# Kernel tuning notes

Measured on AMD Instinct MI355X. Metric: run time of the kernel, lower is better.

Reference implementation:

```python
import jax, jax.numpy as jnp
from jax import lax
import numpy as np

B, CIN, COUT, H, W = 4, 64, 64, 128, 128
K = 3      # kernel size
G = 1      # groups (== offset groups)
PAD = 1
STRIDE = 1


def setup_inputs() -> dict:
    key = jax.random.key(0)
    k1, k2, k3 = jax.random.split(key, 3)
    x = jax.random.normal(k1, (B, CIN, H, W), jnp.float32)
    # offset-predicting conv weight: (2*G*K*K, CIN, K, K); small init like real nets
    w_offset = jax.random.normal(k2, (2 * G * K * K, CIN, K, K), jnp.float32) * 0.01
    # deformable conv weight: (COUT, CIN//G, K, K)
    w_deform = jax.random.normal(k3, (COUT, CIN // G, K, K), jnp.float32) * (1.0 / np.sqrt(CIN * K * K))
    return {"x": x, "w_offset": w_offset, "w_deform": w_deform}


def _deform_conv2d(x, w_offset, w_deform):
    Bn, C, Hi, Wi = x.shape
    K2 = K * K
    Cg = C // G
    # 1) predict offsets with a plain conv
    offset = lax.conv_general_dilated(
        x, w_offset, (STRIDE, STRIDE), [(PAD, PAD), (PAD, PAD)],
        dimension_numbers=("NCHW", "OIHW", "NCHW"))
    Ho, Wo = offset.shape[2], offset.shape[3]
    # torchvision layout: channel 2*(g*K2 + i*K + j) = dy, +1 = dx
    off = offset.reshape(Bn, G, K2, 2, Ho, Wo)
    dy = off[:, :, :, 0]  # (B,G,K2,Ho,Wo)
    dx = off[:, :, :, 1]
    # base sampling grid
    ky = jnp.repeat(jnp.arange(K), K).astype(x.dtype)  # (K2,) kernel row offsets
    kx = jnp.tile(jnp.arange(K), K).astype(x.dtype)    # (K2,) kernel col offsets
    base_y = (jnp.arange(Ho) * STRIDE - PAD).astype(x.dtype)[:, None]   # (Ho,1)
    base_x = (jnp.arange(Wo) * STRIDE - PAD).astype(x.dtype)[None, :]   # (1,Wo)
    py = base_y[None, None, None] + ky[None, None, :, None, None] + dy  # (B,G,K2,Ho,Wo)
    px = base_x[None, None, None] + kx[None, None, :, None, None] + dx
    # 2) bilinear sampling with zero padding outside the image
    y0 = jnp.floor(py)
    x0 = jnp.floor(px)
    ly = py - y0
    lx = px - x0
    y0i = y0.astype(jnp.int32)
    x0i = x0.astype(jnp.int32)
    xr = x.reshape(Bn, G, Cg, Hi, Wi)

    def corner(yi, xi, wgt):
        valid = ((yi >= 0) & (yi < Hi) & (xi >= 0) & (xi < Wi)).astype(x.dtype)
        yc = jnp.clip(yi, 0, Hi - 1)
        xc = jnp.clip(xi, 0, Wi - 1)
        # gather per (batch, group): xg[:, yy, xx] -> (Cg, K2, Ho, Wo)
        g = jax.vmap(jax.vmap(lambda xg, yy, xx: xg[:, yy, xx]))(xr, yc, xc)
        return g * (wgt * valid)[:, :, None]  # broadcast over Cg

    v = (corner(y0i,     x0i,     (1 - ly) * (1 - lx))
         + corner(y0i,     x0i + 1, (1 - ly) * lx)
         + corner(y0i + 1, x0i,     ly * (1 - lx))
         + corner(y0i + 1, x0i + 1, ly * lx))  # (B,G,Cg,K2,Ho,Wo)
    # 3) grouped contraction with the deformable conv weight
    wr = w_deform.reshape(G, COUT // G, Cg, K2)
    out = jnp.einsum('bgckhw,gock->bgohw', v, wr)
    return out.reshape(Bn, COUT, Ho, Wo)


def reference(x, w_offset, w_deform):
    return _deform_conv2d(x, w_offset, w_deform)
```

## Files before the change

kernel.cpp:

```cpp
#include <hip/hip_runtime.h>

#define B_    4
#define CIN_  64
#define COUT_ 64
#define H_    128
#define W_    128
#define HW_   (H_*W_)
#define K2_   9
#define NOFF_ 18

#define PR_   132
#define PC_   136
#define TROWS 5
#define TCOLS 70
#define NSEG  (TROWS * 8 * TCOLS)
#define NSEGP 2816

typedef _Float16 f16x8 __attribute__((ext_vector_type(8)));
typedef float    f32x4 __attribute__((ext_vector_type(4)));

__device__ __forceinline__ f16x8 splat8(float f) {
    _Float16 h = (_Float16)f;
    return (f16x8){h, h, h, h, h, h, h, h};
}
__device__ __forceinline__ f16x8 splat8h(_Float16 h) {
    return (f16x8){h, h, h, h, h, h, h, h};
}
__device__ __forceinline__ _Float16 lo16(unsigned u) {
    return __builtin_bit_cast(_Float16, (unsigned short)(u & 0xffffu));
}
__device__ __forceinline__ _Float16 hi16(unsigned u) {
    return __builtin_bit_cast(_Float16, (unsigned short)(u >> 16));
}

#define NW_B   (COUT_ * 576)
#define NW_OB  (32 * 576)
#define NBORD  (4 * 12544)
__global__ __launch_bounds__(256) void x2h_prep(const float* __restrict__ x,
                                                const float* __restrict__ wd,
                                                const float* __restrict__ wo,
                                                _Float16* __restrict__ hx,
                                                _Float16* __restrict__ wt_b,
                                                _Float16* __restrict__ wt_ob) {
    const int blk = blockIdx.x;
    const int b = blk >> 7, y = blk & 127;
    const int xp = threadIdx.x & 127;
    const int ch = threadIdx.x >> 7;
    const float* xs = x + ((b * CIN_ + ch * 32) * H_ + y) * W_ + xp;
    _Float16* hd = hx + (((size_t)b * PR_ + y + 2) * PC_ + xp + 3) * 64 + ch * 32;

    f16x8 h[4];
    #pragma unroll
    for (int j = 0; j < 4; ++j)
        #pragma unroll
        for (int t = 0; t < 8; ++t)
            h[j][t] = (_Float16)xs[(j * 8 + t) * HW_];
    #pragma unroll
    for (int j = 0; j < 4; ++j)
        *(f16x8*)(hd + j * 8) = h[j];

    const int gid = blk * 256 + threadIdx.x;
    if (gid < NW_B) {
        int blk512 = gid >> 9, w = gid & 511;
        int nl = w >> 5, cc = w & 31;
        int kb = blk512 & 1, t = blk512 >> 1;
        int mb = t / 9, k2 = t - 9 * mb;
        int o = mb * 16 + nl, c = kb * 32 + cc;
        wt_b[gid] = (_Float16)wd[(o * CIN_ + c) * K2_ + k2];
    } else if (gid < NW_B + NW_OB) {
        int u = gid - NW_B;
        int blk512 = u >> 9, w = u & 511;
        int nl = w >> 5, cc = w & 31;
        int kb = blk512 & 1, t = blk512 >> 1;
        int mt = t / 9, k2 = t - 9 * mt;
        int oc = mt * 16 + nl, c = kb * 32 + cc;
        wt_ob[u] = (_Float16)((oc < NOFF_) ? wo[(oc * CIN_ + c) * K2_ + k2] : 0.f);
    } else if (gid < NW_B + NW_OB + NBORD) {
        int s = gid - (NW_B + NW_OB);
        int b2 = s / 12544, u = s % 12544;
        int cs = u & 7, cell = u >> 3;
        int r, c;
        if (cell < 544) {
            int r4 = cell / 136; c = cell % 136;
            r = (r4 < 2) ? r4 : r4 + 128;
        } else {
            int c2 = cell - 544;
            r = 2 + (c2 >> 3);
            int c8 = c2 & 7;
            c = (c8 < 3) ? c8 : c8 + 128;
        }
        *(f16x8*)(hx + (((size_t)b2 * PR_ + r) * PC_ + c) * 64 + cs * 8) = splat8(0.f);
    }
}

__global__ __launch_bounds__(256, 3) void deform_all(const _Float16* __restrict__ hx,
                                                     const _Float16* __restrict__ wt_b,
                                                     const _Float16* __restrict__ wt_ob,
                                                     float* __restrict__ out) {
    __shared__ __align__(16) _Float16 xt[NSEGP * 8];

    const int tid = threadIdx.x;
    int blk = blockIdx.x;
    blk = (blk & 7) * 128 + (blk >> 3);
    const int b   = blk >> 8;
    const int r2  = blk & 255;
    const int oh  = r2 >> 1;
    const int ow0 = (r2 & 1) << 6;

    const _Float16* hrow = hx + (((size_t)b * PR_ + oh) * PC_ + ow0) * 64;
    #pragma unroll
    for (int t = 0; t < NSEGP / 256; ++t) {
        int d  = t * 256 + tid;
        int dc = min(d, NSEG - 1);
        int col = dc % TCOLS;
        int rc  = dc / TCOLS;
        int cs  = rc & 7;
        int r   = rc >> 3;
        const _Float16* src = hrow + ((size_t)r * PC_ + col) * 64 + cs * 8;
        __builtin_amdgcn_global_load_lds(
            (const __attribute__((address_space(1))) void*)src,
            (__attribute__((address_space(3))) void*)(xt + (size_t)d * 8),
            16, 0, 0);
    }

    const int lane = tid & 63;
    const int cq   = tid >> 6;
    const int quad = lane >> 4;
    const int nl   = lane & 15;
    const int pix  = cq * 16 + nl;
    const int ow   = ow0 + pix;

    const _Float16* wob_l = wt_ob + nl * 32 + quad * 8;
    const _Float16* wtb_l = wt_b  + nl * 32 + quad * 8;
    const _Float16* hb    = hx + (size_t)b * (PR_ * PC_ * 64);

    f32x4 oacc[2];
    oacc[0] = (f32x4){0.f, 0.f, 0.f, 0.f};
    oacc[1] = (f32x4){0.f, 0.f, 0.f, 0.f};
    #pragma unroll
    for (int t9 = 0; t9 < 9; ++t9) {
        int ky = t9 / 3, kx = t9 - 3 * (t9 / 3);
        #pragma unroll
        for (int kb = 0; kb < 2; ++kb) {
            f16x8 bfr = *(const f16x8*)(hb + (((oh + ky + 1) * PC_) + (ow + kx + 2)) * 64
                                           + kb * 32 + quad * 8);
            #pragma unroll
            for (int mt = 0; mt < 2; ++mt) {
                f16x8 afr = *(const f16x8*)(wob_l + (((mt * 9 + t9) * 2 + kb) << 9));
                oacc[mt] = __builtin_amdgcn_mfma_f32_16x16x32_f16(afr, bfr, oacc[mt], 0, 0, 0);
            }
        }
    }

    float dyv[9], dxv[9];
    #pragma unroll
    for (int k2 = 0; k2 < 9; ++k2) {
        const int oc0 = 2 * k2;
        const int mt  = oc0 >> 4;
        const int sq  = (oc0 & 15) >> 2;
        const int r0  = oc0 & 3;
        dyv[k2] = __shfl(oacc[mt][r0],     sq * 16 + nl, 64);
        dxv[k2] = __shfl(oacc[mt][r0 + 1], sq * 16 + nl, 64);
    }

    int      A00[9];
    unsigned Wp[9][2];
    int      P0[9];
    unsigned okm = 0, dxm = 0, dym = 0;
    #pragma unroll
    for (int k2 = 0; k2 < 9; ++k2) {
        const int ky = k2 / 3, kx = k2 - 3 * (k2 / 3);
        float py = (float)(oh - 1 + ky) + dyv[k2];
        float px = (float)(ow - 1 + kx) + dxv[k2];
        float y0f = floorf(py), x0f = floorf(px);
        float ly = py - y0f,    lx = px - x0f;
        int   y0 = (int)y0f,    x0 = (int)x0f;
        int   y1 = y0 + 1,      x1 = x0 + 1;

        float wy0 = 1.f - ly, wx0 = 1.f - lx;
        float w00 = wy0 * wx0, w01 = wy0 * lx, w10 = ly * wx0, w11 = ly * lx;

        bool vy0 = (unsigned)y0 < (unsigned)H_;
        bool vy1 = (unsigned)y1 < (unsigned)H_;
        bool vx0 = (unsigned)x0 < (unsigned)W_;
        bool vx1 = (unsigned)x1 < (unsigned)W_;
        if (!(vy0 & vx0)) w00 = 0.f;
        if (!(vy0 & vx1)) w01 = 0.f;
        if (!(vy1 & vx0)) w10 = 0.f;
        if (!(vy1 & vx1)) w11 = 0.f;
        unsigned h00 = (unsigned)__builtin_bit_cast(unsigned short, (_Float16)w00);
        unsigned h01 = (unsigned)__builtin_bit_cast(unsigned short, (_Float16)w01);
        unsigned h10 = (unsigned)__builtin_bit_cast(unsigned short, (_Float16)w10);
        unsigned h11 = (unsigned)__builtin_bit_cast(unsigned short, (_Float16)w11);
        Wp[k2][0] = h00 | (h01 << 16);
        Wp[k2][1] = h10 | (h11 << 16);
        P0[k2] = (y0 & 0xffff) | (x0 << 16);

        int ty0 = y0 - (oh - 2), ty1 = ty0 + 1;
        int tx0 = x0 - (ow0 - 3), tx1 = tx0 + 1;
        bool i00 = (unsigned)ty0 < TROWS && (unsigned)tx0 < TCOLS;
        bool i01 = (unsigned)ty0 < TROWS && (unsigned)tx1 < TCOLS;
        bool i10 = (unsigned)ty1 < TROWS && (unsigned)tx0 < TCOLS;
        bool i11 = (unsigned)ty1 < TROWS && (unsigned)tx1 < TCOLS;
        bool ok = (w00 == 0.f || i00) && (w01 == 0.f || i01) &&
                  (w10 == 0.f || i10) && (w11 == 0.f || i11);
        if (ok) okm |= 1u << k2;

        int tyc0 = min(max(ty0, 0), TROWS - 1), tyc1 = min(max(ty1, 0), TROWS - 1);
        int txc0 = min(max(tx0, 0), TCOLS - 1), txc1 = min(max(tx1, 0), TCOLS - 1);
        if (txc1 != txc0) dxm |= 1u << k2;
        if (tyc1 != tyc0) dym |= 1u << k2;
        A00[k2] = ((tyc0 * 8 + quad) * TCOLS + txc0) * 8;
    }

    __syncthreads();

    f32x4 acc[4];
    #pragma unroll
    for (int mb = 0; mb < 4; ++mb) acc[mb] = (f32x4){0.f, 0.f, 0.f, 0.f};

    const int KB1 = 4 * TCOLS * 8;

    #pragma unroll
    for (int k2 = 0; k2 < 9; ++k2) {
        f16x8 af0[4], af1[4];
        #pragma unroll
        for (int mb = 0; mb < 4; ++mb) {
            af0[mb] = *(const f16x8*)(wtb_l + (((mb * 9 + k2) * 2 + 0) << 9));
            af1[mb] = *(const f16x8*)(wtb_l + (((mb * 9 + k2) * 2 + 1) << 9));
        }

        const int a00 = A00[k2];
        const int a01 = a00 + (int)((dxm >> k2) & 1u) * 8;
        const int a10 = a00 + (int)((dym >> k2) & 1u) * (8 * TCOLS * 8);
        const int a11 = a10 + (a01 - a00);
        f16x8 c00a = *(const f16x8*)&xt[a00], c00b = *(const f16x8*)&xt[a00 + KB1];
        f16x8 c01a = *(const f16x8*)&xt[a01], c01b = *(const f16x8*)&xt[a01 + KB1];
        f16x8 c10a = *(const f16x8*)&xt[a10], c10b = *(const f16x8*)&xt[a10 + KB1];
        f16x8 c11a = *(const f16x8*)&xt[a11], c11b = *(const f16x8*)&xt[a11 + KB1];

        f16x8 W00 = splat8h(lo16(Wp[k2][0])), W01 = splat8h(hi16(Wp[k2][0]));
        f16x8 W10 = splat8h(lo16(Wp[k2][1])), W11 = splat8h(hi16(Wp[k2][1]));

        f16x8 v0 = c00a * W00 + c01a * W01 + c10a * W10 + c11a * W11;
        f16x8 v1 = c00b * W00 + c01b * W01 + c10b * W10 + c11b * W11;

        if (!((okm >> k2) & 1u)) {
            int pk = P0[k2];
            int y0 = (pk << 16) >> 16;
            int x0 = pk >> 16;
            int y0c = min(max(y0, 0), H_ - 1), y1c = min(max(y0 + 1, 0), H_ - 1);
            int x0c = min(max(x0, 0), W_ - 1), x1c = min(max(x0 + 1, 0), W_ - 1);
            const _Float16* hg = hb + quad * 8;
            const _Float16* g00 = hg + (((y0c + 2) * PC_) + x0c + 3) * 64;
            const _Float16* g01 = hg + (((y0c + 2) * PC_) + x1c + 3) * 64;
            const _Float16* g10 = hg + (((y1c + 2) * PC_) + x0c + 3) * 64;
            const _Float16* g11 = hg + (((y1c + 2) * PC_) + x1c + 3) * 64;
            v0 = (*(const f16x8*)g00) * W00 + (*(const f16x8*)g01) * W01 +
                 (*(const f16x8*)g10) * W10 + (*(const f16x8*)g11) * W11;
            v1 = (*(const f16x8*)(g00 + 32)) * W00 + (*(const f16x8*)(g01 + 32)) * W01 +
                 (*(const f16x8*)(g10 + 32)) * W10 + (*(const f16x8*)(g11 + 32)) * W11;
        }

        __builtin_amdgcn_s_setprio(1);
        #pragma unroll
        for (int mb = 0; mb < 4; ++mb) {
            acc[mb] = __builtin_amdgcn_mfma_f32_16x16x32_f16(af0[mb], v0, acc[mb], 0, 0, 0);
            acc[mb] = __builtin_amdgcn_mfma_f32_16x16x32_f16(af1[mb], v1, acc[mb], 0, 0, 0);
        }
        __builtin_amdgcn_s_setprio(0);
    }

    #pragma unroll
    for (int mb = 0; mb < 4; ++mb)
        #pragma unroll
        for (int r = 0; r < 4; ++r) {
            int o = mb * 16 + quad * 4 + r;
            out[(b * COUT_ + o) * HW_ + oh * W_ + ow0 + pix] = acc[mb][r];
        }
}

extern "C" void kernel_launch(void* const* d_in, const int* in_sizes, int n_in,
                              void* d_out, int out_size, void* d_ws, size_t ws_size,
                              hipStream_t stream) {
    const float* x        = (const float*)d_in[0];
    const float* w_offset = (const float*)d_in[1];
    const float* w_deform = (const float*)d_in[2];
    float* out = (float*)d_out;

    _Float16* hx    = (_Float16*)d_ws;
    _Float16* wt_b  = hx + (size_t)B_ * PR_ * PC_ * 64;
    _Float16* wt_ob = wt_b + (size_t)NW_B;

    x2h_prep<<<B_ * H_, 256, 0, stream>>>(x, w_deform, w_offset, hx, wt_b, wt_ob);
    deform_all<<<B_ * H_ * (W_ / 64), 256, 0, stream>>>(hx, wt_b, wt_ob, out);
}
```

Baseline: 116.6 us.

## Halve block size, give each wave two pixel groups, read offset-conv input from LDS

Blocks drop from 256 to 128 threads, so each wave now handles 32 pixels as two 16-pixel groups. The A-fragment weight loads for both the offset conv and the deform contraction are shared across the two groups. The offset conv now reads its B operands from the LDS tile instead of global memory, which requires a barrier right after the async tile load. In exchange it uses more registers per thread and loses the overlap that previously hid the tile load behind the offset conv and coordinate math, and occupancy bounds change.

```diff
diff --git a/kernel.cpp b/kernel.cpp
--- a/kernel.cpp
+++ b/kernel.cpp
@@ -93,7 +93,7 @@
     }
 }
 
-__global__ __launch_bounds__(256, 3) void deform_all(const _Float16* __restrict__ hx,
+__global__ __launch_bounds__(128, 2) void deform_all(const _Float16* __restrict__ hx,
                                                      const _Float16* __restrict__ wt_b,
                                                      const _Float16* __restrict__ wt_ob,
                                                      float* __restrict__ out) {
@@ -109,8 +109,8 @@
 
     const _Float16* hrow = hx + (((size_t)b * PR_ + oh) * PC_ + ow0) * 64;
     #pragma unroll
-    for (int t = 0; t < NSEGP / 256; ++t) {
-        int d  = t * 256 + tid;
+    for (int t = 0; t < NSEGP / 128; ++t) {
+        int d  = t * 128 + tid;
         int dc = min(d, NSEG - 1);
         int col = dc % TCOLS;
         int rc  = dc / TCOLS;
@@ -122,102 +122,109 @@
             (__attribute__((address_space(3))) void*)(xt + (size_t)d * 8),
             16, 0, 0);
     }
+    __syncthreads();
 
     const int lane = tid & 63;
     const int cq   = tid >> 6;
     const int quad = lane >> 4;
     const int nl   = lane & 15;
-    const int pix  = cq * 16 + nl;
-    const int ow   = ow0 + pix;
 
     const _Float16* wob_l = wt_ob + nl * 32 + quad * 8;
     const _Float16* wtb_l = wt_b  + nl * 32 + quad * 8;
     const _Float16* hb    = hx + (size_t)b * (PR_ * PC_ * 64);
 
-    f32x4 oacc[2];
-    oacc[0] = (f32x4){0.f, 0.f, 0.f, 0.f};
-    oacc[1] = (f32x4){0.f, 0.f, 0.f, 0.f};
+    f32x4 oacc[2][2];
+    #pragma unroll
+    for (int mt = 0; mt < 2; ++mt)
+        #pragma unroll
+        for (int pg = 0; pg < 2; ++pg)
+            oacc[mt][pg] = (f32x4){0.f, 0.f, 0.f, 0.f};
     #pragma unroll
     for (int t9 = 0; t9 < 9; ++t9) {
         int ky = t9 / 3, kx = t9 - 3 * (t9 / 3);
         #pragma unroll
         for (int kb = 0; kb < 2; ++kb) {
-            f16x8 bfr = *(const f16x8*)(hb + (((oh + ky + 1) * PC_) + (ow + kx + 2)) * 64
-                                           + kb * 32 + quad * 8);
+            f16x8 afr[2];
             #pragma unroll
-            for (int mt = 0; mt < 2; ++mt) {
-                f16x8 afr = *(const f16x8*)(wob_l + (((mt * 9 + t9) * 2 + kb) << 9));
-                oacc[mt] = __builtin_amdgcn_mfma_f32_16x16x32_f16(afr, bfr, oacc[mt], 0, 0, 0);
+            for (int mt = 0; mt < 2; ++mt)
+                afr[mt] = *(const f16x8*)(wob_l + (((mt * 9 + t9) * 2 + kb) << 9));
+            #pragma unroll
+            for (int pg = 0; pg < 2; ++pg) {
+                const int pix = cq * 32 + pg * 16 + nl;
+                f16x8 bfr = *(const f16x8*)&xt[((((ky + 1) * 8) + kb * 4 + quad) * TCOLS + pix + kx + 2) * 8];
+                #pragma unroll
+                for (int mt = 0; mt < 2; ++mt)
+                    oacc[mt][pg] = __builtin_amdgcn_mfma_f32_16x16x32_f16(afr[mt], bfr, oacc[mt][pg], 0, 0, 0);
             }
         }
     }
 
-    float dyv[9], dxv[9];
-    #pragma unroll
-    for (int k2 = 0; k2 < 9; ++k2) {
-        const int oc0 = 2 * k2;
-        const int mt  = oc0 >> 4;
-        const int sq  = (oc0 & 15) >> 2;
-        const int r0  = oc0 & 3;
-        dyv[k2] = __shfl(oacc[mt][r0],     sq * 16 + nl, 64);
-        dxv[k2] = __shfl(oacc[mt][r0 + 1], sq * 16 + nl, 64);
-    }
-
-    int      A00[9];
-    unsigned Wp[9][2];
-    int      P0[9];
-    unsigned okm = 0, dxm = 0, dym = 0;
-    #pragma unroll
-    for (int k2 = 0; k2 < 9; ++k2) {
-        const int ky = k2 / 3, kx = k2 - 3 * (k2 / 3);
-        float py = (float)(oh - 1 + ky) + dyv[k2];
-        float px = (float)(ow - 1 + kx) + dxv[k2];
-        float y0f = floorf(py), x0f = floorf(px);
-        float ly = py - y0f,    lx = px - x0f;
-        int   y0 = (int)y0f,    x0 = (int)x0f;
-        int   y1 = y0 + 1,      x1 = x0 + 1;
-
-        float wy0 = 1.f - ly, wx0 = 1.f - lx;
-        float w00 = wy0 * wx0, w01 = wy0 * lx, w10 = ly * wx0, w11 = ly * lx;
-
-        bool vy0 = (unsigned)y0 < (unsigned)H_;
-        bool vy1 = (unsigned)y1 < (unsigned)H_;
-        bool vx0 = (unsigned)x0 < (unsigned)W_;
-        bool vx1 = (unsigned)x1 < (unsigned)W_;
-        if (!(vy0 & vx0)) w00 = 0.f;
-        if (!(vy0 & vx1)) w01 = 0.f;
-        if (!(vy1 & vx0)) w10 = 0.f;
-        if (!(vy1 & vx1)) w11 = 0.f;
-        unsigned h00 = (unsigned)__builtin_bit_cast(unsigned short, (_Float16)w00);
-        unsigned h01 = (unsigned)__builtin_bit_cast(unsigned short, (_Float16)w01);
-        unsigned h10 = (unsigned)__builtin_bit_cast(unsigned short, (_Float16)w10);
-        unsigned h11 = (unsigned)__builtin_bit_cast(unsigned short, (_Float16)w11);
-        Wp[k2][0] = h00 | (h01 << 16);
-        Wp[k2][1] = h10 | (h11 << 16);
-        P0[k2] = (y0 & 0xffff) | (x0 << 16);
-
-        int ty0 = y0 - (oh - 2), ty1 = ty0 + 1;
-        int tx0 = x0 - (ow0 - 3), tx1 = tx0 + 1;
-        bool i00 = (unsigned)ty0 < TROWS && (unsigned)tx0 < TCOLS;
-        bool i01 = (unsigned)ty0 < TROWS && (unsigned)tx1 < TCOLS;
-        bool i10 = (unsigned)ty1 < TROWS && (unsigned)tx0 < TCOLS;
-        bool i11 = (unsigned)ty1 < TROWS && (unsigned)tx1 < TCOLS;
-        bool ok = (w00 == 0.f || i00) && (w01 == 0.f || i01) &&
-                  (w10 == 0.f || i10) && (w11 == 0.f || i11);
-        if (ok) okm |= 1u << k2;
-
-        int tyc0 = min(max(ty0, 0), TROWS - 1), tyc1 = min(max(ty1, 0), TROWS - 1);
-        int txc0 = min(max(tx0, 0), TCOLS - 1), txc1 = min(max(tx1, 0), TCOLS - 1);
-        if (txc1 != txc0) dxm |= 1u << k2;
-        if (tyc1 != tyc0) dym |= 1u << k2;
-        A00[k2] = ((tyc0 * 8 + quad) * TCOLS + txc0) * 8;
-    }
-
-    __syncthreads();
-
-    f32x4 acc[4];
-    #pragma unroll
-    for (int mb = 0; mb < 4; ++mb) acc[mb] = (f32x4){0.f, 0.f, 0.f, 0.f};
+    int      A00[2][9];
+    unsigned Wp[2][9][2];
+    int      P0[2][9];
+    unsigned okm[2] = {0, 0}, dxm[2] = {0, 0}, dym[2] = {0, 0};
+    #pragma unroll
+    for (int pg = 0; pg < 2; ++pg) {
+        const int ow = ow0 + cq * 32 + pg * 16 + nl;
+        #pragma unroll
+        for (int k2 = 0; k2 < 9; ++k2) {
+            const int oc0 = 2 * k2;
+            const int mt  = oc0 >> 4;
+            const int sq  = (oc0 & 15) >> 2;
+            const int r0  = oc0 & 3;
+            float dy = __shfl(oacc[mt][pg][r0],     sq * 16 + nl, 64);
+            float dx = __shfl(oacc[mt][pg][r0 + 1], sq * 16 + nl, 64);
+
+            const int ky = k2 / 3, kx = k2 - 3 * (k2 / 3);
+            float py = (float)(oh - 1 + ky) + dy;
+            float px = (float)(ow - 1 + kx) + dx;
+            float y0f = floorf(py), x0f = floorf(px);
+            float ly = py - y0f,    lx = px - x0f;
+            int   y0 = (int)y0f,    x0 = (int)x0f;
+            int   y1 = y0 + 1,      x1 = x0 + 1;
+
+            float wy0 = 1.f - ly, wx0 = 1.f - lx;
+            float w00 = wy0 * wx0, w01 = wy0 * lx, w10 = ly * wx0, w11 = ly * lx;
+
+            bool vy0 = (unsigned)y0 < (unsigned)H_;
+            bool vy1 = (unsigned)y1 < (unsigned)H_;
+            bool vx0 = (unsigned)x0 < (unsigned)W_;
+            bool vx1 = (unsigned)x1 < (unsigned)W_;
+            if (!(vy0 & vx0)) w00 = 0.f;
+            if (!(vy0 & vx1)) w01 = 0.f;
+            if (!(vy1 & vx0)) w10 = 0.f;
+            if (!(vy1 & vx1)) w11 = 0.f;
+            unsigned h00 = (unsigned)__builtin_bit_cast(unsigned short, (_Float16)w00);
+            unsigned h01 = (unsigned)__builtin_bit_cast(unsigned short, (_Float16)w01);
+            unsigned h10 = (unsigned)__builtin_bit_cast(unsigned short, (_Float16)w10);
+            unsigned h11 = (unsigned)__builtin_bit_cast(unsigned short, (_Float16)w11);
+            Wp[pg][k2][0] = h00 | (h01 << 16);
+            Wp[pg][k2][1] = h10 | (h11 << 16);
+            P0[pg][k2] = (y0 & 0xffff) | (x0 << 16);
+
+            int ty0 = y0 - (oh - 2), ty1 = ty0 + 1;
+            int tx0 = x0 - (ow0 - 3), tx1 = tx0 + 1;
+            bool i00 = (unsigned)ty0 < TROWS && (unsigned)tx0 < TCOLS;
+            bool i01 = (unsigned)ty0 < TROWS && (unsigned)tx1 < TCOLS;
+            bool i10 = (unsigned)ty1 < TROWS && (unsigned)tx0 < TCOLS;
+            bool i11 = (unsigned)ty1 < TROWS && (unsigned)tx1 < TCOLS;
+            bool ok = (w00 == 0.f || i00) && (w01 == 0.f || i01) &&
+                      (w10 == 0.f || i10) && (w11 == 0.f || i11);
+            if (ok) okm[pg] |= 1u << k2;
+
+            int tyc0 = min(max(ty0, 0), TROWS - 1), tyc1 = min(max(ty1, 0), TROWS - 1);
+            int txc0 = min(max(tx0, 0), TCOLS - 1), txc1 = min(max(tx1, 0), TCOLS - 1);
+            if (txc1 != txc0) dxm[pg] |= 1u << k2;
+            if (tyc1 != tyc0) dym[pg] |= 1u << k2;
+            A00[pg][k2] = ((tyc0 * 8 + quad) * TCOLS + txc0) * 8;
+        }
+    }
+
+    f32x4 acc[2][4];
+    #pragma unroll
+    for (int pg = 0; pg < 2; ++pg)
+        #pragma unroll
+        for (int mb = 0; mb < 4; ++mb) acc[pg][mb] = (f32x4){0.f, 0.f, 0.f, 0.f};
 
     const int KB1 = 4 * TCOLS * 8;
 
@@ -230,54 +237,59 @@
             af1[mb] = *(const f16x8*)(wtb_l + (((mb * 9 + k2) * 2 + 1) << 9));
         }
 
-        const int a00 = A00[k2];
-        const int a01 = a00 + (int)((dxm >> k2) & 1u) * 8;
-        const int a10 = a00 + (int)((dym >> k2) & 1u) * (8 * TCOLS * 8);
-        const int a11 = a10 + (a01 - a00);
-        f16x8 c00a = *(const f16x8*)&xt[a00], c00b = *(const f16x8*)&xt[a00 + KB1];
-        f16x8 c01a = *(const f16x8*)&xt[a01], c01b = *(const f16x8*)&xt[a01 + KB1];
-        f16x8 c10a = *(const f16x8*)&xt[a10], c10b = *(const f16x8*)&xt[a10 + KB1];
-        f16x8 c11a = *(const f16x8*)&xt[a11], c11b = *(const f16x8*)&xt[a11 + KB1];
-
-        f16x8 W00 = splat8h(lo16(Wp[k2][0])), W01 = splat8h(hi16(Wp[k2][0]));
-        f16x8 W10 = splat8h(lo16(Wp[k2][1])), W11 = splat8h(hi16(Wp[k2][1]));
-
-        f16x8 v0 = c00a * W00 + c01a * W01 + c10a * W10 + c11a * W11;
-        f16x8 v1 = c00b * W00 + c01b * W01 + c10b * W10 + c11b * W11;
-
-        if (!((okm >> k2) & 1u)) {
-            int pk = P0[k2];
-            int y0 = (pk << 16) >> 16;
-            int x0 = pk >> 16;
-            int y0c = min(max(y0, 0), H_ - 1), y1c = min(max(y0 + 1, 0), H_ - 1);
-            int x0c = min(max(x0, 0), W_ - 1), x1c = min(max(x0 + 1, 0), W_ - 1);
-            const _Float16* hg = hb + quad * 8;
-            const _Float16* g00 = hg + (((y0c + 2) * PC_) + x0c + 3) * 64;
-            const _Float16* g01 = hg + (((y0c + 2) * PC_) + x1c + 3) * 64;
-            const _Float16* g10 = hg + (((y1c + 2) * PC_) + x0c + 3) * 64;
-            const _Float16* g11 = hg + (((y1c + 2) * PC_) + x1c + 3) * 64;
-            v0 = (*(const f16x8*)g00) * W00 + (*(const f16x8*)g01) * W01 +
-                 (*(const f16x8*)g10) * W10 + (*(const f16x8*)g11) * W11;
-            v1 = (*(const f16x8*)(g00 + 32)) * W00 + (*(const f16x8*)(g01 + 32)) * W01 +
-                 (*(const f16x8*)(g10 + 32)) * W10 + (*(const f16x8*)(g11 + 32)) * W11;
-        }
-
-        __builtin_amdgcn_s_setprio(1);
-        #pragma unroll
-        for (int mb = 0; mb < 4; ++mb) {
-            acc[mb] = __builtin_amdgcn_mfma_f32_16x16x32_f16(af0[mb], v0, acc[mb], 0, 0, 0);
-            acc[mb] = __builtin_amdgcn_mfma_f32_16x16x32_f16(af1[mb], v1, acc[mb], 0, 0, 0);
-        }
-        __builtin_amdgcn_s_setprio(0);
-    }
-
-    #pragma unroll
-    for (int mb = 0; mb < 4; ++mb)
-        #pragma unroll
-        for (int r = 0; r < 4; ++r) {
-            int o = mb * 16 + quad * 4 + r;
-            out[(b * COUT_ + o) * HW_ + oh * W_ + ow0 + pix] = acc[mb][r];
-        }
+        #pragma unroll
+        for (int pg = 0; pg < 2; ++pg) {
+            const int a00 = A00[pg][k2];
+            const int a01 = a00 + (int)((dxm[pg] >> k2) & 1u) * 8;
+            const int a10 = a00 + (int)((dym[pg] >> k2) & 1u) * (8 * TCOLS * 8);
+            const int a11 = a10 + (a01 - a00);
+            f16x8 c00a = *(const f16x8*)&xt[a00], c00b = *(const f16x8*)&xt[a00 + KB1];
+            f16x8 c01a = *(const f16x8*)&xt[a01], c01b = *(const f16x8*)&xt[a01 + KB1];
+            f16x8 c10a = *(const f16x8*)&xt[a10], c10b = *(const f16x8*)&xt[a10 + KB1];
+            f16x8 c11a = *(const f16x8*)&xt[a11], c11b = *(const f16x8*)&xt[a11 + KB1];
+
+            f16x8 W00 = splat8h(lo16(Wp[pg][k2][0])), W01 = splat8h(hi16(Wp[pg][k2][0]));
+            f16x8 W10 = splat8h(lo16(Wp[pg][k2][1])), W11 = splat8h(hi16(Wp[pg][k2][1]));
+
+            f16x8 v0 = c00a * W00 + c01a * W01 + c10a * W10 + c11a * W11;
+            f16x8 v1 = c00b * W00 + c01b * W01 + c10b * W10 + c11b * W11;
+
+            if (!((okm[pg] >> k2) & 1u)) {
+                int pk = P0[pg][k2];
+                int y0 = (pk << 16) >> 16;
+                int x0 = pk >> 16;
+                int y0c = min(max(y0, 0), H_ - 1), y1c = min(max(y0 + 1, 0), H_ - 1);
+                int x0c = min(max(x0, 0), W_ - 1), x1c = min(max(x0 + 1, 0), W_ - 1);
+                const _Float16* hg = hb + quad * 8;
+                const _Float16* g00 = hg + (((y0c + 2) * PC_) + x0c + 3) * 64;
+                const _Float16* g01 = hg + (((y0c + 2) * PC_) + x1c + 3) * 64;
+                const _Float16* g10 = hg + (((y1c + 2) * PC_) + x0c + 3) * 64;
+                const _Float16* g11 = hg + (((y1c + 2) * PC_) + x1c + 3) * 64;
+                v0 = (*(const f16x8*)g00) * W00 + (*(const f16x8*)g01) * W01 +
+                     (*(const f16x8*)g10) * W10 + (*(const f16x8*)g11) * W11;
+                v1 = (*(const f16x8*)(g00 + 32)) * W00 + (*(const f16x8*)(g01 + 32)) * W01 +
+                     (*(const f16x8*)(g10 + 32)) * W10 + (*(const f16x8*)(g11 + 32)) * W11;
+            }
+
+            __builtin_amdgcn_s_setprio(1);
+            #pragma unroll
+            for (int mb = 0; mb < 4; ++mb) {
+                acc[pg][mb] = __builtin_amdgcn_mfma_f32_16x16x32_f16(af0[mb], v0, acc[pg][mb], 0, 0, 0);
+                acc[pg][mb] = __builtin_amdgcn_mfma_f32_16x16x32_f16(af1[mb], v1, acc[pg][mb], 0, 0, 0);
+            }
+            __builtin_amdgcn_s_setprio(0);
+        }
+    }
+
+    #pragma unroll
+    for (int pg = 0; pg < 2; ++pg)
+        #pragma unroll
+        for (int mb = 0; mb < 4; ++mb)
+            #pragma unroll
+            for (int r = 0; r < 4; ++r) {
+                int o = mb * 16 + quad * 4 + r;
+                out[(b * COUT_ + o) * HW_ + oh * W_ + ow0 + cq * 32 + pg * 16 + nl] = acc[pg][mb][r];
+            }
 }
 
 extern "C" void kernel_launch(void* const* d_in, const int* in_sizes, int n_in,
@@ -293,5 +305,5 @@
     _Float16* wt_ob = wt_b + (size_t)NW_B;
 
     x2h_prep<<<B_ * H_, 256, 0, stream>>>(x, w_deform, w_offset, hx, wt_b, wt_ob);
-    deform_all<<<B_ * H_ * (W_ / 64), 256, 0, stream>>>(hx, wt_b, wt_ob, out);
-}
+    deform_all<<<B_ * H_ * (W_ / 64), 128, 0, stream>>>(hx, wt_b, wt_ob, out);
+}
```

After: 108.0 us (median of 2 runs). -7.4%, faster.

## Split offset conv and sampling metadata into a separate kernel

Applied to the files above, without the earlier changes.

Moves the offset-predicting convolution and bilinear metadata computation into a new kernel that writes packed per-pixel records (weights, tile address bits, fallback coords) to workspace. The main kernel then loads these records instead of computing them, which lowers register pressure and removes the MFMA offset conv from its critical path. In exchange it adds a kernel launch and a global-memory round trip for the metadata, and the offset conv no longer overlaps with the LDS tile load.

```diff
diff --git a/kernel.cpp b/kernel.cpp
--- a/kernel.cpp
+++ b/kernel.cpp
@@ -18,6 +18,7 @@
 
 typedef _Float16 f16x8 __attribute__((ext_vector_type(8)));
 typedef float    f32x4 __attribute__((ext_vector_type(4)));
+typedef unsigned u32x4 __attribute__((ext_vector_type(4)));
 
 __device__ __forceinline__ f16x8 splat8(float f) {
     _Float16 h = (_Float16)f;
@@ -93,10 +94,109 @@
     }
 }
 
-__global__ __launch_bounds__(256, 3) void deform_all(const _Float16* __restrict__ hx,
-                                                     const _Float16* __restrict__ wt_b,
+__global__ __launch_bounds__(256, 4) void oconv_meta(const _Float16* __restrict__ hx,
                                                      const _Float16* __restrict__ wt_ob,
-                                                     float* __restrict__ out) {
+                                                     u32x4* __restrict__ meta) {
+    int blk = blockIdx.x;
+    blk = (blk & 7) * 128 + (blk >> 3);
+    const int b   = blk >> 8;
+    const int r2  = blk & 255;
+    const int oh  = r2 >> 1;
+    const int ow0 = (r2 & 1) << 6;
+
+    const int tid  = threadIdx.x;
+    const int lane = tid & 63;
+    const int cq   = tid >> 6;
+    const int quad = lane >> 4;
+    const int nl   = lane & 15;
+    const int pix  = cq * 16 + nl;
+    const int ow   = ow0 + pix;
+
+    const _Float16* wob_l = wt_ob + nl * 32 + quad * 8;
+    const _Float16* hb    = hx + (size_t)b * (PR_ * PC_ * 64);
+
+    f32x4 oacc[2];
+    oacc[0] = (f32x4){0.f, 0.f, 0.f, 0.f};
+    oacc[1] = (f32x4){0.f, 0.f, 0.f, 0.f};
+    #pragma unroll
+    for (int t9 = 0; t9 < 9; ++t9) {
+        int ky = t9 / 3, kx = t9 - 3 * (t9 / 3);
+        #pragma unroll
+        for (int kb = 0; kb < 2; ++kb) {
+            f16x8 bfr = *(const f16x8*)(hb + (((oh + ky + 1) * PC_) + (ow + kx + 2)) * 64
+                                           + kb * 32 + quad * 8);
+            #pragma unroll
+            for (int mt = 0; mt < 2; ++mt) {
+                f16x8 afr = *(const f16x8*)(wob_l + (((mt * 9 + t9) * 2 + kb) << 9));
+                oacc[mt] = __builtin_amdgcn_mfma_f32_16x16x32_f16(afr, bfr, oacc[mt], 0, 0, 0);
+            }
+        }
+    }
+
+    #pragma unroll
+    for (int k2 = 0; k2 < 9; ++k2) {
+        const int oc0 = 2 * k2;
+        const int mt  = oc0 >> 4;
+        const int sq  = (oc0 & 15) >> 2;
+        const int r0  = oc0 & 3;
+        float dy = __shfl(oacc[mt][r0],     sq * 16 + nl, 64);
+        float dx = __shfl(oacc[mt][r0 + 1], sq * 16 + nl, 64);
+
+        const int ky = k2 / 3, kx = k2 - 3 * (k2 / 3);
+        float py = (float)(oh - 1 + ky) + dy;
+        float px = (float)(ow - 1 + kx) + dx;
+        float y0f = floorf(py), x0f = floorf(px);
+        float ly = py - y0f,    lx = px - x0f;
+        int   y0 = (int)y0f,    x0 = (int)x0f;
+        int   y1 = y0 + 1,      x1 = x0 + 1;
+
+        float wy0 = 1.f - ly, wx0 = 1.f - lx;
+        float w00 = wy0 * wx0, w01 = wy0 * lx, w10 = ly * wx0, w11 = ly * lx;
+
+        bool vy0 = (unsigned)y0 < (unsigned)H_;
+        bool vy1 = (unsigned)y1 < (unsigned)H_;
+        bool vx0 = (unsigned)x0 < (unsigned)W_;
+        bool vx1 = (unsigned)x1 < (unsigned)W_;
+        if (!(vy0 & vx0)) w00 = 0.f;
+        if (!(vy0 & vx1)) w01 = 0.f;
+        if (!(vy1 & vx0)) w10 = 0.f;
+        if (!(vy1 & vx1)) w11 = 0.f;
+        unsigned h00 = (unsigned)__builtin_bit_cast(unsigned short, (_Float16)w00);
+        unsigned h01 = (unsigned)__builtin_bit_cast(unsigned short, (_Float16)w01);
+        unsigned h10 = (unsigned)__builtin_bit_cast(unsigned short, (_Float16)w10);
+        unsigned h11 = (unsigned)__builtin_bit_cast(unsigned short, (_Float16)w11);
+
+        int ty0 = y0 - (oh - 2), ty1 = ty0 + 1;
+        int tx0 = x0 - (ow0 - 3), tx1 = tx0 + 1;
+        bool i00 = (unsigned)ty0 < TROWS && (unsigned)tx0 < TCOLS;
+        bool i01 = (unsigned)ty0 < TROWS && (unsigned)tx1 < TCOLS;
+        bool i10 = (unsigned)ty1 < TROWS && (unsigned)tx0 < TCOLS;
+        bool i11 = (unsigned)ty1 < TROWS && (unsigned)tx1 < TCOLS;
+        bool ok = (w00 == 0.f || i00) && (w01 == 0.f || i01) &&
+                  (w10 == 0.f || i10) && (w11 == 0.f || i11);
+
+        int tyc0 = min(max(ty0, 0), TROWS - 1), tyc1 = min(max(ty1, 0), TROWS - 1);
+        int txc0 = min(max(tx0, 0), TCOLS - 1), txc1 = min(max(tx1, 0), TCOLS - 1);
+        unsigned s = (unsigned)((tyc0 * 8 * TCOLS + txc0) * 8);
+        unsigned u = s | ((txc1 != txc0) ? (1u << 15) : 0u)
+                       | ((tyc1 != tyc0) ? (1u << 16) : 0u)
+                       | (ok ? (1u << 17) : 0u);
+
+        if (quad == 0) {
+            u32x4 rec;
+            rec[0] = h00 | (h01 << 16);
+            rec[1] = h10 | (h11 << 16);
+            rec[2] = u;
+            rec[3] = (unsigned)((y0 & 0xffff) | (x0 << 16));
+            meta[((size_t)blk * 9 + k2) * 64 + pix] = rec;
+        }
+    }
+}
+
+__global__ __launch_bounds__(256, 3) void deform_main(const _Float16* __restrict__ hx,
+                                                      const _Float16* __restrict__ wt_b,
+                                                      const u32x4* __restrict__ meta,
+                                                      float* __restrict__ out) {
     __shared__ __align__(16) _Float16 xt[NSEGP * 8];
 
     const int tid = threadIdx.x;
@@ -128,92 +228,16 @@
     const int quad = lane >> 4;
     const int nl   = lane & 15;
     const int pix  = cq * 16 + nl;
-    const int ow   = ow0 + pix;
-
-    const _Float16* wob_l = wt_ob + nl * 32 + quad * 8;
-    const _Float16* wtb_l = wt_b  + nl * 32 + quad * 8;
+
+    u32x4 m[9];
+    #pragma unroll
+    for (int k2 = 0; k2 < 9; ++k2)
+        m[k2] = meta[((size_t)blk * 9 + k2) * 64 + pix];
+
+    __syncthreads();
+
+    const _Float16* wtb_l = wt_b + nl * 32 + quad * 8;
     const _Float16* hb    = hx + (size_t)b * (PR_ * PC_ * 64);
-
-    f32x4 oacc[2];
-    oacc[0] = (f32x4){0.f, 0.f, 0.f, 0.f};
-    oacc[1] = (f32x4){0.f, 0.f, 0.f, 0.f};
-    #pragma unroll
-    for (int t9 = 0; t9 < 9; ++t9) {
-        int ky = t9 / 3, kx = t9 - 3 * (t9 / 3);
-        #pragma unroll
-        for (int kb = 0; kb < 2; ++kb) {
-            f16x8 bfr = *(const f16x8*)(hb + (((oh + ky + 1) * PC_) + (ow + kx + 2)) * 64
-                                           + kb * 32 + quad * 8);
-            #pragma unroll
-            for (int mt = 0; mt < 2; ++mt) {
-                f16x8 afr = *(const f16x8*)(wob_l + (((mt * 9 + t9) * 2 + kb) << 9));
-                oacc[mt] = __builtin_amdgcn_mfma_f32_16x16x32_f16(afr, bfr, oacc[mt], 0, 0, 0);
-            }
-        }
-    }
-
-    float dyv[9], dxv[9];
-    #pragma unroll
-    for (int k2 = 0; k2 < 9; ++k2) {
-        const int oc0 = 2 * k2;
-        const int mt  = oc0 >> 4;
-        const int sq  = (oc0 & 15) >> 2;
-        const int r0  = oc0 & 3;
-        dyv[k2] = __shfl(oacc[mt][r0],     sq * 16 + nl, 64);
-        dxv[k2] = __shfl(oacc[mt][r0 + 1], sq * 16 + nl, 64);
-    }
-
-    int      A00[9];
-    unsigned Wp[9][2];
-    int      P0[9];
-    unsigned okm = 0, dxm = 0, dym = 0;
-    #pragma unroll
-    for (int k2 = 0; k2 < 9; ++k2) {
-        const int ky = k2 / 3, kx = k2 - 3 * (k2 / 3);
-        float py = (float)(oh - 1 + ky) + dyv[k2];
-        float px = (float)(ow - 1 + kx) + dxv[k2];
-        float y0f = floorf(py), x0f = floorf(px);
-        float ly = py - y0f,    lx = px - x0f;
-        int   y0 = (int)y0f,    x0 = (int)x0f;
-        int   y1 = y0 + 1,      x1 = x0 + 1;
-
-        float wy0 = 1.f - ly, wx0 = 1.f - lx;
-        float w00 = wy0 * wx0, w01 = wy0 * lx, w10 = ly * wx0, w11 = ly * lx;
-
-        bool vy0 = (unsigned)y0 < (unsigned)H_;
-        bool vy1 = (unsigned)y1 < (unsigned)H_;
-        bool vx0 = (unsigned)x0 < (unsigned)W_;
-        bool vx1 = (unsigned)x1 < (unsigned)W_;
-        if (!(vy0 & vx0)) w00 = 0.f;
-        if (!(vy0 & vx1)) w01 = 0.f;
-        if (!(vy1 & vx0)) w10 = 0.f;
-        if (!(vy1 & vx1)) w11 = 0.f;
-        unsigned h00 = (unsigned)__builtin_bit_cast(unsigned short, (_Float16)w00);
-        unsigned h01 = (unsigned)__builtin_bit_cast(unsigned short, (_Float16)w01);
-        unsigned h10 = (unsigned)__builtin_bit_cast(unsigned short, (_Float16)w10);
-        unsigned h11 = (unsigned)__builtin_bit_cast(unsigned short, (_Float16)w11);
-        Wp[k2][0] = h00 | (h01 << 16);
-        Wp[k2][1] = h10 | (h11 << 16);
-        P0[k2] = (y0 & 0xffff) | (x0 << 16);
-
-        int ty0 = y0 - (oh - 2), ty1 = ty0 + 1;
-        int tx0 = x0 - (ow0 - 3), tx1 = tx0 + 1;
-        bool i00 = (unsigned)ty0 < TROWS && (unsigned)tx0 < TCOLS;
-        bool i01 = (unsigned)ty0 < TROWS && (unsigned)tx1 < TCOLS;
-        bool i10 = (unsigned)ty1 < TROWS && (unsigned)tx0 < TCOLS;
-        bool i11 = (unsigned)ty1 < TROWS && (unsigned)tx1 < TCOLS;
-        bool ok = (w00 == 0.f || i00) && (w01 == 0.f || i01) &&
-                  (w10 == 0.f || i10) && (w11 == 0.f || i11);
-        if (ok) okm |= 1u << k2;
-
-        int tyc0 = min(max(ty0, 0), TROWS - 1), tyc1 = min(max(ty1, 0), TROWS - 1);
-        int txc0 = min(max(tx0, 0), TCOLS - 1), txc1 = min(max(tx1, 0), TCOLS - 1);
-        if (txc1 != txc0) dxm |= 1u << k2;
-        if (tyc1 != tyc0) dym |= 1u << k2;
-        A00[k2] = ((tyc0 * 8 + quad) * TCOLS + txc0) * 8;
-    }
-
-    __syncthreads();
 
     f32x4 acc[4];
     #pragma unroll
@@ -230,23 +254,25 @@
             af1[mb] = *(const f16x8*)(wtb_l + (((mb * 9 + k2) * 2 + 1) << 9));
         }
 
-        const int a00 = A00[k2];
-        const int a01 = a00 + (int)((dxm >> k2) & 1u) * 8;
-        const int a10 = a00 + (int)((dym >> k2) & 1u) * (8 * TCOLS * 8);
+        const unsigned u = m[k2][2];
+        const int a00 = (int)(u & 0x7fffu) + quad * (TCOLS * 8);
+        const int a01 = a00 + (int)((u >> 15) & 1u) * 8;
+        const int a10 = a00 + (int)((u >> 16) & 1u) * (8 * TCOLS * 8);
         const int a11 = a10 + (a01 - a00);
+
         f16x8 c00a = *(const f16x8*)&xt[a00], c00b = *(const f16x8*)&xt[a00 + KB1];
         f16x8 c01a = *(const f16x8*)&xt[a01], c01b = *(const f16x8*)&xt[a01 + KB1];
         f16x8 c10a = *(const f16x8*)&xt[a10], c10b = *(const f16x8*)&xt[a10 + KB1];
         f16x8 c11a = *(const f16x8*)&xt[a11], c11b = *(const f16x8*)&xt[a11 + KB1];
 
-        f16x8 W00 = splat8h(lo16(Wp[k2][0])), W01 = splat8h(hi16(Wp[k2][0]));
-        f16x8 W10 = splat8h(lo16(Wp[k2][1])), W11 = splat8h(hi16(Wp[k2][1]));
+        f16x8 W00 = splat8h(lo16(m[k2][0])), W01 = splat8h(hi16(m[k2][0]));
+        f16x8 W10 = splat8h(lo16(m[k2][1])), W11 = splat8h(hi16(m[k2][1]));
 
         f16x8 v0 = c00a * W00 + c01a * W01 + c10a * W10 + c11a * W11;
         f16x8 v1 = c00b * W00 + c01b * W01 + c10b * W10 + c11b * W11;
 
-        if (!((okm >> k2) & 1u)) {
-            int pk = P0[k2];
+        if (!((u >> 17) & 1u)) {
+            int pk = (int)m[k2][3];
             int y0 = (pk << 16) >> 16;
             int x0 = pk >> 16;
             int y0c = min(max(y0, 0), H_ - 1), y1c = min(max(y0 + 1, 0), H_ - 1);
@@ -291,7 +317,9 @@
     _Float16* hx    = (_Float16*)d_ws;
     _Float16* wt_b  = hx + (size_t)B_ * PR_ * PC_ * 64;
     _Float16* wt_ob = wt_b + (size_t)NW_B;
+    u32x4*    meta  = (u32x4*)(wt_ob + NW_OB);
 
     x2h_prep<<<B_ * H_, 256, 0, stream>>>(x, w_deform, w_offset, hx, wt_b, wt_ob);
-    deform_all<<<B_ * H_ * (W_ / 64), 256, 0, stream>>>(hx, wt_b, wt_ob, out);
-}
+    oconv_meta<<<B_ * H_ * (W_ / 64), 256, 0, stream>>>(hx, wt_ob, meta);
+    deform_main<<<B_ * H_ * (W_ / 64), 256, 0, stream>>>(hx, wt_b, meta, out);
+}
```

Result: slower. 122.1 us (+4.7%).
